# Performance work log

Measured on AMD Instinct MI355X. Metric: run time of the kernel, lower is better.

The kernel has to match this reference:

```python
import jax, jax.numpy as jnp
import numpy as np

N_FREQS = 6  # PositionEmbedding N_freqs when embedding=='pe'

def _pe(x):
    freqs = (2.0 ** jnp.arange(N_FREQS)).astype(x.dtype)
    fx = x * freqs  # [B,Q,N_FREQS]
    sc = jnp.stack([jnp.sin(fx), jnp.cos(fx)], axis=-1).reshape(fx.shape[0], fx.shape[1], 2 * N_FREQS)
    return jnp.concatenate([x, sc], axis=-1)

def _mlp(h, W1, b1, W2, b2, W3, b3):
    h = jax.nn.relu(h @ W1 + b1)
    h = jax.nn.relu(h @ W2 + b2)
    return h @ W3 + b3

def setup_inputs() -> dict:
    key = jax.random.key(0)
    B, Q, N, D, H = 4, 65536, 8192, 16, 128
    ks = jax.random.split(key, 6)
    coord = jax.random.uniform(ks[0], (B, Q, 1), minval=-1.0, maxval=1.0, dtype=jnp.float32)
    latent = jax.random.normal(ks[1], (B, N, D), dtype=jnp.float32)
    in_dim = (1 + 2 * N_FREQS) + 3 * D  # pe(rel_coord) ++ unfolded feat = 13 + 48 = 61
    def init(k, shp, fan):
        return (jax.random.normal(k, shp, dtype=jnp.float32) / np.float32(np.sqrt(fan)))
    W1 = init(ks[2], (in_dim, H), in_dim); b1 = jnp.zeros((H,), jnp.float32)
    W2 = init(ks[3], (H, H), H);          b2 = jnp.zeros((H,), jnp.float32)
    W3 = init(ks[4], (H, 1), H);          b3 = jnp.zeros((1,), jnp.float32)
    return dict(coord=coord, latent=latent, W1=W1, b1=b1, W2=W2, b2=b2, W3=W3, b3=b3)

def reference(coord, latent, W1, b1, W2, b2, W3, b3):
    B, Q, _ = coord.shape
    N = latent.shape[1]
    # feat_unfold: concat shifted-prev / self / shifted-next along feature dim -> [B,N,3D]
    prev = jnp.concatenate([latent[:, :1], latent[:, :-1]], axis=1)
    nxt = jnp.concatenate([latent[:, 1:], latent[:, -1:]], axis=1)
    feat = jnp.concatenate([prev, latent, nxt], axis=-1)
    # make_coord grid: cell centers in [-1,1]
    grid = (-1.0 + (2.0 * jnp.arange(N, dtype=coord.dtype) + 1.0) / N)
    rx = 1.0 / N           # 2/num_latents/2
    eps_shift = 1e-6
    preds, areas = [], []
    for vx in (-2.0, 0.0):  # eval path vx_lst
        c = jnp.clip(coord + vx * rx + eps_shift, -1.0 + 1e-6, 1.0 - 1e-6)
        idx = jnp.clip(jnp.searchsorted(grid, c[..., 0]), 0, N - 1)  # [B,Q]
        q_coord = grid[idx][..., None]                               # [B,Q,1]
        q_feat = jnp.take_along_axis(feat, idx[..., None], axis=1)   # [B,Q,3D]
        rel = (coord - q_coord) * N                                  # scaled rel coord
        area = jnp.abs(rel[..., 0]) + 1e-9                           # [B,Q]
        inp = jnp.concatenate([_pe(rel), q_feat], axis=-1)           # [B,Q,61]
        preds.append(_mlp(inp, W1, b1, W2, b2, W3, b3))              # [B,Q,1]
        areas.append(area)
    tot = areas[0] + areas[1]
    # local_ensemble: swap areas before weighting
    ret = preds[0] * (areas[1] / tot)[..., None] + preds[1] * (areas[0] / tot)[..., None]
    return ret
```

## Files before the change

### kernel.cpp

```cpp
#include <hip/hip_runtime.h>
#include <hip/hip_bf16.h>

typedef short s8v __attribute__((ext_vector_type(8)));
typedef float f4v __attribute__((ext_vector_type(4)));
typedef unsigned u4v __attribute__((ext_vector_type(4)));

__device__ __forceinline__ unsigned short f2bf(float x) {
  unsigned u = __builtin_bit_cast(unsigned, x);
  u += 0x7fffu + ((u >> 16) & 1u);
  return (unsigned short)(u >> 16);
}
#if __has_builtin(__builtin_amdgcn_cvt_pk_bf16_f32)
__device__ __forceinline__ unsigned pk2(float a, float b) {
  return __builtin_bit_cast(unsigned, __builtin_amdgcn_cvt_pk_bf16_f32(a, b));
}
#else
__device__ __forceinline__ unsigned pk2(float a, float b) {
  unsigned ua = __builtin_bit_cast(unsigned, a) + 0x8000u;
  unsigned ub = __builtin_bit_cast(unsigned, b) + 0x8000u;
  return __builtin_amdgcn_perm(ub, ua, 0x07060302u);
}
#endif

__device__ __forceinline__ void g2lds16(const void* g, void* l) {
  __builtin_amdgcn_global_load_lds(
      (const __attribute__((address_space(1))) unsigned*)g,
      (__attribute__((address_space(3))) unsigned*)l, 16, 0, 0);
}

__global__ void prep_kernel(const float* __restrict__ W1, const float* __restrict__ b1,
                            const float* __restrict__ W2, const float* __restrict__ latent,
                            unsigned short* __restrict__ wsW) {
  int e = blockIdx.x * 256 + threadIdx.x;
  if (e < 8192) {
    int frag = e >> 9, rem = e & 511, lane = rem >> 3, j = rem & 7;
    int h = frag >> 1, ks = frag & 1;
    int q4 = lane >> 4, l15 = lane & 15;
    int k = ks * 32 + q4 * 8 + j;
    int n = h * 16 + l15;
    float v;
    if (k < 13) v = W1[k * 128 + n];
    else if (k == 13) v = b1[n];
    else if (k < 16) v = 0.0f;
    else v = W1[(k - 3) * 128 + n];
    wsW[e] = f2bf(v);
  } else if (e < 24576) {
    int e2 = e - 8192;
    int frag = e2 >> 9, rem = e2 & 511, lane = rem >> 3, j = rem & 7;
    int h2 = frag >> 2, ks = frag & 3;
    int q4 = lane >> 4, l15 = lane & 15;
    int kd = (j < 4) ? (32 * ks + 4 * q4 + j) : (32 * ks + 16 + 4 * q4 + (j - 4));
    int n = h2 * 16 + l15;
    wsW[e] = f2bf(W2[kd * 128 + n]);
  } else {
    int i = e - 24576;
    float4 v = ((const float4*)latent)[i];
    uint2 o;
    o.x = pk2(v.x, v.y);
    o.y = pk2(v.z, v.w);
    ((uint2*)(wsW + 24576))[i] = o;
  }
}

__global__ __launch_bounds__(256, 2) void lisagon_main(
    const float* __restrict__ coord, const unsigned short* __restrict__ latbf,
    const unsigned short* __restrict__ W1f, const unsigned short* __restrict__ W2f,
    const float* __restrict__ b2, const float* __restrict__ W3,
    const float* __restrict__ b3, float* __restrict__ out) {
  __shared__ __align__(16) unsigned short W2s[16384];
  __shared__ __align__(16) unsigned PE[2][256][4];
  __shared__ __align__(16) float BW[256];

  const int t = threadIdx.x;
  const int lane = t & 63, wv = t >> 6;
  const int l15 = lane & 15, q4 = lane >> 4;
  const int bid = ((blockIdx.x & 7) >> 1) * 512 + ((blockIdx.x >> 3) << 1) + (blockIdx.x & 1);

#pragma unroll
  for (int it = 0; it < 8; it++) {
    int off = (it * 4 + wv) * 1024;
    g2lds16((const char*)W2f + off + lane * 16, (char*)W2s + off);
  }
  if (t < 64) {
    ((float4*)BW)[t] = (t < 32) ? ((const float4*)b2)[t] : ((const float4*)W3)[t - 32];
  }
  const s8v* W1fv = (const s8v*)W1f;
  s8v W1r[16];
#pragma unroll
  for (int i = 0; i < 16; i++) W1r[i] = W1fv[i * 64 + lane];

  int idx;
  float area;
  {
    const int Rg = bid * 256 + t;
    const int gq = Rg >> 1, p = Rg & 1;
    const float co = coord[gq];
    float c = (co + (p ? 0.0f : -0.000244140625f)) + 1e-6f;
    c = fminf(fmaxf(c, -1.0f + 1e-6f), 1.0f - 1e-6f);
    double u = ((double)c * 8192.0 + 8191.0) * 0.5;
    idx = (int)ceil(u);
    idx = min(max(idx, 0), 8191);
    float qc = ((float)(2 * idx + 1) - 8192.0f) * (1.0f / 8192.0f);
    float rel = (co - qc) * 8192.0f;
    area = fabsf(rel) + 1e-9f;
    float v[16];
    v[0] = rel;
    float f = rel;
#pragma unroll
    for (int i = 0; i < 6; i++) {
      v[1 + 2 * i] = __sinf(f);
      v[2 + 2 * i] = __cosf(f);
      f = f + f;
    }
    v[13] = 1.0f;
    v[14] = 0.0f; v[15] = 0.0f;
    uint4 q0, q1;
    q0.x = pk2(v[0], v[1]);   q0.y = pk2(v[2], v[3]);
    q0.z = pk2(v[4], v[5]);   q0.w = pk2(v[6], v[7]);
    q1.x = pk2(v[8], v[9]);   q1.y = pk2(v[10], v[11]);
    q1.z = pk2(v[12], v[13]); q1.w = pk2(v[14], v[15]);
    ((uint4*)PE[0])[t] = q0;
    ((uint4*)PE[1])[t] = q1;
  }

  const size_t bbase = (size_t)(bid >> 9) * (8192 * 16);
  const uint4* latv4 = (const uint4*)(latbf + bbase);
  const int rbase = wv * 64;
  s8v Bf[2][4];
#pragma unroll
  for (int rt = 0; rt < 4; rt++) {
    int srcl = rt * 16 + l15;
    int sidx = __shfl(idx, srcl, 64);
    int rp = max(sidx - 1, 0), rn = min(sidx + 1, 8191);
    int c = q4 & 1;
    uint4 g0 = latv4[rp * 2 + c];
    uint4 g1 = latv4[(q4 < 2 ? sidx : rn) * 2 + c];
    uint4 pe = ((const uint4*)PE[c])[rbase + srcl];
    uint4 b0;
    b0.x = q4 < 2 ? pe.x : g0.x;  b0.y = q4 < 2 ? pe.y : g0.y;
    b0.z = q4 < 2 ? pe.z : g0.z;  b0.w = q4 < 2 ? pe.w : g0.w;
    Bf[0][rt] = __builtin_bit_cast(s8v, b0);
    Bf[1][rt] = __builtin_bit_cast(s8v, g1);
  }

  u4v bbv[4][4];
#pragma unroll
  for (int h = 0; h < 8; h++) {
    f4v a[4];
#pragma unroll
    for (int rt = 0; rt < 4; rt++) a[rt] = (f4v){0.f, 0.f, 0.f, 0.f};
#pragma unroll
    for (int ks = 0; ks < 2; ks++) {
#pragma unroll
      for (int rt = 0; rt < 4; rt++)
        a[rt] = __builtin_amdgcn_mfma_f32_16x16x32_bf16(W1r[h * 2 + ks], Bf[ks][rt],
                                                        a[rt], 0, 0, 0);
    }
#pragma unroll
    for (int rt = 0; rt < 4; rt++) {
      bbv[rt][h >> 1][2 * (h & 1)]     = pk2(fmaxf(a[rt][0], 0.f), fmaxf(a[rt][1], 0.f));
      bbv[rt][h >> 1][2 * (h & 1) + 1] = pk2(fmaxf(a[rt][2], 0.f), fmaxf(a[rt][3], 0.f));
    }
  }

  __syncthreads();

  const s8v* W2sv = (const s8v*)W2s;
  float s[4] = {0.f, 0.f, 0.f, 0.f};
#pragma unroll
  for (int h2 = 0; h2 < 8; h2++) {
    f4v a2[4];
    f4v b2v = ((const f4v*)BW)[h2 * 4 + q4];
#pragma unroll
    for (int rt = 0; rt < 4; rt++) a2[rt] = b2v;
#pragma unroll
    for (int ks = 0; ks < 4; ks++) {
      s8v Af = W2sv[(h2 * 4 + ks) * 64 + lane];
#pragma unroll
      for (int rt = 0; rt < 4; rt++)
        a2[rt] = __builtin_amdgcn_mfma_f32_16x16x32_bf16(
            Af, __builtin_bit_cast(s8v, bbv[rt][ks]), a2[rt], 0, 0, 0);
    }
    float4 w3v = ((const float4*)(BW + 128))[h2 * 4 + q4];
#pragma unroll
    for (int rt = 0; rt < 4; rt++) {
      s[rt] += fmaxf(a2[rt][0], 0.f) * w3v.x;
      s[rt] += fmaxf(a2[rt][1], 0.f) * w3v.y;
      s[rt] += fmaxf(a2[rt][2], 0.f) * w3v.z;
      s[rt] += fmaxf(a2[rt][3], 0.f) * w3v.w;
    }
  }

  const float b3s = b3[0];
#pragma unroll
  for (int rt = 0; rt < 4; rt++) {
    float pred = s[rt];
    pred += __shfl_xor(pred, 16, 64);
    pred += __shfl_xor(pred, 32, 64);
    pred += b3s;
    float other = __shfl_xor(pred, 1, 64);
    float a0 = __shfl(area, rt * 16 + l15, 64);
    float a1 = __shfl(area, rt * 16 + l15 + 1, 64);
    if (q4 == 0 && (l15 & 1) == 0) {
      int row0 = rbase + rt * 16 + l15;
      float tot = a0 + a1;
      out[(bid * 256 + row0) >> 1] = pred * (a1 / tot) + other * (a0 / tot);
    }
  }
}

extern "C" void kernel_launch(void* const* d_in, const int* in_sizes, int n_in,
                              void* d_out, int out_size, void* d_ws, size_t ws_size,
                              hipStream_t stream) {
  const float* coord  = (const float*)d_in[0];
  const float* latent = (const float*)d_in[1];
  const float* W1 = (const float*)d_in[2];
  const float* b1 = (const float*)d_in[3];
  const float* W2 = (const float*)d_in[4];
  const float* b2 = (const float*)d_in[5];
  const float* W3 = (const float*)d_in[6];
  const float* b3 = (const float*)d_in[7];
  float* out = (float*)d_out;
  unsigned short* wsW = (unsigned short*)d_ws;

  prep_kernel<<<608, 256, 0, stream>>>(W1, b1, W2, latent, wsW);
  lisagon_main<<<2048, 256, 0, stream>>>(coord, wsW + 24576, wsW, wsW + 8192,
                                         b2, W3, b3, out);
}
```

Baseline: 95.16 us.

## Use single-wave blocks and read weights from global instead of LDS

The main kernel now launches 64-thread single-wave blocks, four times as many as before. W2, b2 and W3 are no longer staged into shared memory; each MFMA step reads its W2 fragment straight from global/L2. W1 fragments are also loaded per step rather than kept resident in registers, and the block barrier and launch bounds are removed. The aim is to drop the LDS staging, the barrier and the register pressure so occupancy rises, at the cost of repeated global weight loads that depend on cache hits.

```diff
diff --git a/kernel.cpp b/kernel.cpp
--- a/kernel.cpp
+++ b/kernel.cpp
@@ -21,12 +21,6 @@
   return __builtin_amdgcn_perm(ub, ua, 0x07060302u);
 }
 #endif
-
-__device__ __forceinline__ void g2lds16(const void* g, void* l) {
-  __builtin_amdgcn_global_load_lds(
-      (const __attribute__((address_space(1))) unsigned*)g,
-      (__attribute__((address_space(3))) unsigned*)l, 16, 0, 0);
-}
 
 __global__ void prep_kernel(const float* __restrict__ W1, const float* __restrict__ b1,
                             const float* __restrict__ W2, const float* __restrict__ latent,
@@ -62,37 +56,22 @@
   }
 }
 
-__global__ __launch_bounds__(256, 2) void lisagon_main(
+__global__ void lisagon_main(
     const float* __restrict__ coord, const unsigned short* __restrict__ latbf,
     const unsigned short* __restrict__ W1f, const unsigned short* __restrict__ W2f,
     const float* __restrict__ b2, const float* __restrict__ W3,
     const float* __restrict__ b3, float* __restrict__ out) {
-  __shared__ __align__(16) unsigned short W2s[16384];
-  __shared__ __align__(16) unsigned PE[2][256][4];
-  __shared__ __align__(16) float BW[256];
+  __shared__ __align__(16) unsigned PE[2][64][4];
 
   const int t = threadIdx.x;
-  const int lane = t & 63, wv = t >> 6;
+  const int lane = t;
   const int l15 = lane & 15, q4 = lane >> 4;
-  const int bid = ((blockIdx.x & 7) >> 1) * 512 + ((blockIdx.x >> 3) << 1) + (blockIdx.x & 1);
-
-#pragma unroll
-  for (int it = 0; it < 8; it++) {
-    int off = (it * 4 + wv) * 1024;
-    g2lds16((const char*)W2f + off + lane * 16, (char*)W2s + off);
-  }
-  if (t < 64) {
-    ((float4*)BW)[t] = (t < 32) ? ((const float4*)b2)[t] : ((const float4*)W3)[t - 32];
-  }
-  const s8v* W1fv = (const s8v*)W1f;
-  s8v W1r[16];
-#pragma unroll
-  for (int i = 0; i < 16; i++) W1r[i] = W1fv[i * 64 + lane];
+  const int bid = ((blockIdx.x & 7) >> 1) * 2048 + ((blockIdx.x >> 3) << 1) + (blockIdx.x & 1);
 
   int idx;
   float area;
   {
-    const int Rg = bid * 256 + t;
+    const int Rg = bid * 64 + t;
     const int gq = Rg >> 1, p = Rg & 1;
     const float co = coord[gq];
     float c = (co + (p ? 0.0f : -0.000244140625f)) + 1e-6f;
@@ -123,9 +102,8 @@
     ((uint4*)PE[1])[t] = q1;
   }
 
-  const size_t bbase = (size_t)(bid >> 9) * (8192 * 16);
+  const size_t bbase = (size_t)(bid >> 11) * (8192 * 16);
   const uint4* latv4 = (const uint4*)(latbf + bbase);
-  const int rbase = wv * 64;
   s8v Bf[2][4];
 #pragma unroll
   for (int rt = 0; rt < 4; rt++) {
@@ -135,7 +113,7 @@
     int c = q4 & 1;
     uint4 g0 = latv4[rp * 2 + c];
     uint4 g1 = latv4[(q4 < 2 ? sidx : rn) * 2 + c];
-    uint4 pe = ((const uint4*)PE[c])[rbase + srcl];
+    uint4 pe = ((const uint4*)PE[c])[srcl];
     uint4 b0;
     b0.x = q4 < 2 ? pe.x : g0.x;  b0.y = q4 < 2 ? pe.y : g0.y;
     b0.z = q4 < 2 ? pe.z : g0.z;  b0.w = q4 < 2 ? pe.w : g0.w;
@@ -143,6 +121,7 @@
     Bf[1][rt] = __builtin_bit_cast(s8v, g1);
   }
 
+  const s8v* W1fv = (const s8v*)W1f;
   u4v bbv[4][4];
 #pragma unroll
   for (int h = 0; h < 8; h++) {
@@ -151,10 +130,10 @@
     for (int rt = 0; rt < 4; rt++) a[rt] = (f4v){0.f, 0.f, 0.f, 0.f};
 #pragma unroll
     for (int ks = 0; ks < 2; ks++) {
+      s8v w1 = W1fv[(h * 2 + ks) * 64 + lane];
 #pragma unroll
       for (int rt = 0; rt < 4; rt++)
-        a[rt] = __builtin_amdgcn_mfma_f32_16x16x32_bf16(W1r[h * 2 + ks], Bf[ks][rt],
-                                                        a[rt], 0, 0, 0);
+        a[rt] = __builtin_amdgcn_mfma_f32_16x16x32_bf16(w1, Bf[ks][rt], a[rt], 0, 0, 0);
     }
 #pragma unroll
     for (int rt = 0; rt < 4; rt++) {
@@ -163,25 +142,23 @@
     }
   }
 
-  __syncthreads();
-
-  const s8v* W2sv = (const s8v*)W2s;
+  const s8v* W2fv = (const s8v*)W2f;
   float s[4] = {0.f, 0.f, 0.f, 0.f};
 #pragma unroll
   for (int h2 = 0; h2 < 8; h2++) {
     f4v a2[4];
-    f4v b2v = ((const f4v*)BW)[h2 * 4 + q4];
+    f4v b2v = ((const f4v*)b2)[h2 * 4 + q4];
 #pragma unroll
     for (int rt = 0; rt < 4; rt++) a2[rt] = b2v;
 #pragma unroll
     for (int ks = 0; ks < 4; ks++) {
-      s8v Af = W2sv[(h2 * 4 + ks) * 64 + lane];
+      s8v Af = W2fv[(h2 * 4 + ks) * 64 + lane];
 #pragma unroll
       for (int rt = 0; rt < 4; rt++)
         a2[rt] = __builtin_amdgcn_mfma_f32_16x16x32_bf16(
             Af, __builtin_bit_cast(s8v, bbv[rt][ks]), a2[rt], 0, 0, 0);
     }
-    float4 w3v = ((const float4*)(BW + 128))[h2 * 4 + q4];
+    float4 w3v = ((const float4*)W3)[h2 * 4 + q4];
 #pragma unroll
     for (int rt = 0; rt < 4; rt++) {
       s[rt] += fmaxf(a2[rt][0], 0.f) * w3v.x;
@@ -202,9 +179,9 @@
     float a0 = __shfl(area, rt * 16 + l15, 64);
     float a1 = __shfl(area, rt * 16 + l15 + 1, 64);
     if (q4 == 0 && (l15 & 1) == 0) {
-      int row0 = rbase + rt * 16 + l15;
+      int row0 = rt * 16 + l15;
       float tot = a0 + a1;
-      out[(bid * 256 + row0) >> 1] = pred * (a1 / tot) + other * (a0 / tot);
+      out[(bid * 64 + row0) >> 1] = pred * (a1 / tot) + other * (a0 / tot);
     }
   }
 }
@@ -224,6 +201,6 @@
   unsigned short* wsW = (unsigned short*)d_ws;
 
   prep_kernel<<<608, 256, 0, stream>>>(W1, b1, W2, latent, wsW);
-  lisagon_main<<<2048, 256, 0, stream>>>(coord, wsW + 24576, wsW, wsW + 8192,
-                                         b2, W3, b3, out);
-}
+  lisagon_main<<<8192, 64, 0, stream>>>(coord, wsW + 24576, wsW, wsW + 8192,
+                                        b2, W3, b3, out);
+}
```

Result: slower. 140.4 us (+47.6%).
